# Optimization experiments

Hardware: AMD Instinct MI355X
Metric: run time of the kernel (lower is better)

The kernel has to match this reference:

```python
import jax, jax.numpy as jnp
import numpy as np
import math

TAU_PLUS = 20.0
TAU_MINUS = 20.0
A_PLUS = 0.01
A_MINUS = 0.01
W_MAX = 1.0
W_MIN = 0.0
TARGET_RATE = 0.1
HOMEO = 0.001
RATE_ALPHA = 0.01
DT = 1.0


def setup_inputs() -> dict:
    key = jax.random.key(0)
    k1, k2, k3, k4 = jax.random.split(key, 4)
    B, PRE, POST = 1024, 4096, 4096
    return {
        "pre_spikes": jax.random.uniform(k1, (B, PRE), dtype=jnp.float32),
        "post_spikes": jax.random.uniform(k2, (B, POST), dtype=jnp.float32),
        "weights": jax.random.uniform(k3, (POST, PRE), dtype=jnp.float32) * 0.5,
        "pre_trace": jnp.zeros((B, PRE), dtype=jnp.float32),
        "post_trace": jnp.zeros((B, POST), dtype=jnp.float32),
        "running_rate": jax.random.uniform(k4, (POST,), dtype=jnp.float32) * 0.2,
    }


def reference(pre_spikes, post_spikes, weights, pre_trace, post_trace, running_rate):
    B = pre_spikes.shape[0]
    # trace decay
    pre_tr = pre_trace * math.exp(-DT / TAU_PLUS)
    post_tr = post_trace * math.exp(-DT / TAU_MINUS)
    # STDP weight update (learn=True, auto_scale=False)
    dw_plus = A_PLUS * jnp.einsum('bp,bq->pq', post_spikes, pre_tr) / B
    dw_minus = -A_MINUS * jnp.einsum('bp,bq->pq', post_tr, pre_spikes) / B
    dw_homeo = -HOMEO * (running_rate - TARGET_RATE)[:, None]
    new_weights = jnp.clip(weights + dw_plus + dw_minus + dw_homeo, W_MIN, W_MAX)
    # homeostatic rate EMA
    batch_rate = post_spikes.mean(axis=0)
    new_rate = running_rate * (1.0 - RATE_ALPHA) + RATE_ALPHA * batch_rate
    # trace update
    new_pre_trace = pre_tr + pre_spikes
    new_post_trace = post_tr + post_spikes
    # postsynaptic current with updated weights
    current = pre_spikes @ new_weights.T  # (B, POST)
    return current, new_weights, new_pre_trace, new_post_trace, new_rate
```

## Files before the change

### kernel.cpp

```cpp
#include <hip/hip_runtime.h>
#include <hip/hip_fp8.h>

typedef __attribute__((ext_vector_type(8))) short short8;
typedef __attribute__((ext_vector_type(4))) float floatx4;
typedef __attribute__((ext_vector_type(8))) int int8v;
typedef __attribute__((ext_vector_type(4))) int int4v;

#define LDS_PTR(x) ((__attribute__((address_space(3))) unsigned int*)(x))
#define GLB_PTR(x) ((const __attribute__((address_space(1))) unsigned int*)(x))

__device__ __forceinline__ unsigned short f2bf(float f) {
    unsigned int u = __float_as_uint(f);
    unsigned int r = (u + 0x7FFFu + ((u >> 16) & 1u)) >> 16;
    return (unsigned short)r;
}
__device__ __forceinline__ unsigned char f2fp8(float f) {
    __hip_fp8_e4m3 v(f);
    return (unsigned char)v.__x;
}
__device__ __forceinline__ float fp82f(unsigned int u) {
    __hip_fp8_e4m3 v;
    v.__x = (__hip_fp8_storage_t)(u & 0xFF);
    return (float)v;
}

__global__ __launch_bounds__(256) void prep_post_kernel(
    const float* __restrict__ S, const float* __restrict__ T,
    float* __restrict__ traceOut, unsigned char* __restrict__ At,
    int C, int K2, int Bsz, float dp)
{
    __shared__ float sT[64][65];
    __shared__ float tT[64][65];
    const int t = threadIdx.x;
    const int r0 = blockIdx.y * 64, c0 = blockIdx.x * 64;
#pragma unroll
    for (int i = 0; i < 4; ++i) {
        int rl = (t >> 4) + i * 16;
        int cl = (t & 15) * 4;
        size_t g = (size_t)(r0 + rl) * C + c0 + cl;
        float4 s4 = *(const float4*)&S[g];
        float4 t4 = *(const float4*)&T[g];
        float4 o;
        o.x = fmaf(t4.x, dp, s4.x); o.y = fmaf(t4.y, dp, s4.y);
        o.z = fmaf(t4.z, dp, s4.z); o.w = fmaf(t4.w, dp, s4.w);
        *(float4*)&traceOut[g] = o;
        sT[rl][cl + 0] = s4.x; sT[rl][cl + 1] = s4.y;
        sT[rl][cl + 2] = s4.z; sT[rl][cl + 3] = s4.w;
        tT[rl][cl + 0] = t4.x; tT[rl][cl + 1] = t4.y;
        tT[rl][cl + 2] = t4.z; tT[rl][cl + 3] = t4.w;
    }
    __syncthreads();
#pragma unroll
    for (int i = 0; i < 4; ++i) {
        int cl = (t >> 4) + i * 16;
        int rl = (t & 15) * 4;
        uchar4 a, b;
        a.x = f2fp8(sT[rl + 0][cl]); a.y = f2fp8(sT[rl + 1][cl]);
        a.z = f2fp8(sT[rl + 2][cl]); a.w = f2fp8(sT[rl + 3][cl]);
        b.x = f2fp8(tT[rl + 0][cl]); b.y = f2fp8(tT[rl + 1][cl]);
        b.z = f2fp8(tT[rl + 2][cl]); b.w = f2fp8(tT[rl + 3][cl]);
        *(uchar4*)&At[(size_t)(c0 + cl) * K2 + r0 + rl] = a;
        *(uchar4*)&At[(size_t)(c0 + cl) * K2 + Bsz + r0 + rl] = b;
    }
}

__global__ __launch_bounds__(256) void prep_pre_kernel(
    const float* __restrict__ S, const float* __restrict__ T,
    float* __restrict__ traceOut, unsigned char* __restrict__ Bt,
    unsigned short* __restrict__ preBf,
    int C, int K2, int Bsz, float dp)
{
    __shared__ float sT[64][65];
    __shared__ float tT[64][65];
    const int t = threadIdx.x;
    const int r0 = blockIdx.y * 64, c0 = blockIdx.x * 64;
#pragma unroll
    for (int i = 0; i < 4; ++i) {
        int rl = (t >> 4) + i * 16;
        int cl = (t & 15) * 4;
        size_t g = (size_t)(r0 + rl) * C + c0 + cl;
        float4 s4 = *(const float4*)&S[g];
        float4 t4 = *(const float4*)&T[g];
        float4 o;
        o.x = fmaf(t4.x, dp, s4.x); o.y = fmaf(t4.y, dp, s4.y);
        o.z = fmaf(t4.z, dp, s4.z); o.w = fmaf(t4.w, dp, s4.w);
        *(float4*)&traceOut[g] = o;
        ushort4 pb = { f2bf(s4.x), f2bf(s4.y), f2bf(s4.z), f2bf(s4.w) };
        *(ushort4*)&preBf[g] = pb;
        sT[rl][cl + 0] = s4.x; sT[rl][cl + 1] = s4.y;
        sT[rl][cl + 2] = s4.z; sT[rl][cl + 3] = s4.w;
        tT[rl][cl + 0] = t4.x; tT[rl][cl + 1] = t4.y;
        tT[rl][cl + 2] = t4.z; tT[rl][cl + 3] = t4.w;
    }
    __syncthreads();
#pragma unroll
    for (int i = 0; i < 4; ++i) {
        int cl = (t >> 4) + i * 16;
        int rl = (t & 15) * 4;
        uchar4 a, b;
        a.x = f2fp8(tT[rl + 0][cl]); a.y = f2fp8(tT[rl + 1][cl]);
        a.z = f2fp8(tT[rl + 2][cl]); a.w = f2fp8(tT[rl + 3][cl]);
        b.x = f2fp8(-sT[rl + 0][cl]); b.y = f2fp8(-sT[rl + 1][cl]);
        b.z = f2fp8(-sT[rl + 2][cl]); b.w = f2fp8(-sT[rl + 3][cl]);
        *(uchar4*)&Bt[(size_t)(c0 + cl) * K2 + r0 + rl] = a;
        *(uchar4*)&Bt[(size_t)(c0 + cl) * K2 + Bsz + r0 + rl] = b;
    }
}

__global__ __launch_bounds__(256) void rate_kernel(
    const unsigned char* __restrict__ At, const float* __restrict__ rr,
    float* __restrict__ new_rate, int K2, int Bsz)
{
    const int w = threadIdx.x >> 6, l = threadIdx.x & 63;
    const int p = blockIdx.x * 4 + w;
    const unsigned char* row = At + (size_t)p * K2;
    float s = 0.f;
    for (int k = l * 16; k < Bsz; k += 1024) {
        int4v v = *(const int4v*)&row[k];
#pragma unroll
        for (int wd = 0; wd < 4; ++wd) {
            unsigned int u = (unsigned int)v[wd];
            s += fp82f(u) + fp82f(u >> 8) + fp82f(u >> 16) + fp82f(u >> 24);
        }
    }
#pragma unroll
    for (int off = 32; off > 0; off >>= 1) s += __shfl_xor(s, off, 64);
    if (l == 0)
        new_rate[p] = rr[p] * 0.99f + 0.01f * (s / (float)Bsz);
}

__global__ __launch_bounds__(256) void dw_fp8_kernel(
    const unsigned char* __restrict__ A, const unsigned char* __restrict__ B,
    int K, int N, float s,
    const float* __restrict__ Wold, const float* __restrict__ rr,
    float* __restrict__ outF, unsigned short* __restrict__ outBf)
{
    constexpr int BM = 128, BN = 128, BK = 128;
    __shared__ unsigned char lA[2][BM * BK];
    __shared__ unsigned char lB[2][BN * BK];

    const int t = threadIdx.x;
    const int l = t & 63;
    const int w = t >> 6;
    const int wm = w >> 1, wn = w & 1;
    const int bm = blockIdx.y, bn = blockIdx.x;

    floatx4 acc[4][4] = {};

    auto stage = [&](int buf, int k0) {
#pragma unroll
        for (int i = 0; i < 4; ++i) {
            int ci = i * 256 + t;
            int r = ci >> 3, sc = ci & 7;
            int g = sc ^ (r & 7);
            const unsigned char* gpA = A + (size_t)(bm * BM + r) * K + k0 + g * 16;
            __builtin_amdgcn_global_load_lds(GLB_PTR(gpA),
                LDS_PTR(&lA[buf][ci * 16]), 16, 0, 0);
            const unsigned char* gpB = B + (size_t)(bn * BN + r) * K + k0 + g * 16;
            __builtin_amdgcn_global_load_lds(GLB_PTR(gpB),
                LDS_PTR(&lB[buf][ci * 16]), 16, 0, 0);
        }
    };

    stage(0, 0);
    __syncthreads();

    const int nT = K / BK;
    int cur = 0;
    for (int tt = 0; tt < nT; ++tt) {
        if (tt + 1 < nT) stage(cur ^ 1, (tt + 1) * BK);

        const int c = l >> 4;
        const int m = l & 15;
        int8v af[4], bf[4];
#pragma unroll
        for (int i = 0; i < 4; ++i) {
            int ra = wm * 64 + i * 16 + m;
            int s0 = (2 * c) ^ (ra & 7), s1 = (2 * c + 1) ^ (ra & 7);
            int4v lo = *(const int4v*)&lA[cur][ra * BK + s0 * 16];
            int4v hi = *(const int4v*)&lA[cur][ra * BK + s1 * 16];
            af[i][0] = lo[0]; af[i][1] = lo[1]; af[i][2] = lo[2]; af[i][3] = lo[3];
            af[i][4] = hi[0]; af[i][5] = hi[1]; af[i][6] = hi[2]; af[i][7] = hi[3];
        }
#pragma unroll
        for (int j = 0; j < 4; ++j) {
            int rb = wn * 64 + j * 16 + m;
            int s0 = (2 * c) ^ (rb & 7), s1 = (2 * c + 1) ^ (rb & 7);
            int4v lo = *(const int4v*)&lB[cur][rb * BK + s0 * 16];
            int4v hi = *(const int4v*)&lB[cur][rb * BK + s1 * 16];
            bf[j][0] = lo[0]; bf[j][1] = lo[1]; bf[j][2] = lo[2]; bf[j][3] = lo[3];
            bf[j][4] = hi[0]; bf[j][5] = hi[1]; bf[j][6] = hi[2]; bf[j][7] = hi[3];
        }
#pragma unroll
        for (int i = 0; i < 4; ++i)
#pragma unroll
            for (int j = 0; j < 4; ++j)
                acc[i][j] = __builtin_amdgcn_mfma_scale_f32_16x16x128_f8f6f4(
                    af[i], bf[j], acc[i][j], 0, 0, 0, 0x7f, 0, 0x7f);

        asm volatile("s_waitcnt vmcnt(0)" ::: "memory");
        __builtin_amdgcn_s_barrier();
        cur ^= 1;
    }

    const int pBase = bm * BM + wm * 64;
    const int qBase = bn * BN + wn * 64;
#pragma unroll
    for (int i = 0; i < 4; ++i) {
#pragma unroll
        for (int r = 0; r < 4; ++r) {
            const int p = pBase + i * 16 + (l >> 4) * 4 + r;
            const float hp = -0.001f * (rr[p] - 0.1f);
#pragma unroll
            for (int j = 0; j < 4; ++j) {
                const int q = qBase + j * 16 + (l & 15);
                const size_t idx = (size_t)p * N + q;
                float v = fmaf(s, acc[i][j][r], Wold[idx] + hp);
                v = fminf(fmaxf(v, 0.f), 1.f);
                outF[idx] = v;
                outBf[idx] = f2bf(v);
            }
        }
    }
}

template <int BM, int BN>
__global__ __launch_bounds__(256) void mfma_gemm_bt(
    const unsigned short* __restrict__ A,
    const unsigned short* __restrict__ Bm,
    int K, int N, float* __restrict__ outF)
{
    constexpr int BK = 32;
    constexpr int FI = BM / 32;
    constexpr int FJ = BN / 32;
    __shared__ unsigned short lA[2][BM * BK];
    __shared__ unsigned short lB[2][BN * BK];

    const int t = threadIdx.x;
    const int l = t & 63;
    const int w = t >> 6;
    const int wm = w >> 1, wn = w & 1;
    const int bm = blockIdx.y, bn = blockIdx.x;

    const int srow = t >> 2;
    const int sc = t & 3;
    const int gc = sc ^ ((srow >> 1) & 3);
    const int skc = sc * 8;
    const int gkc = gc * 8;

    floatx4 acc[FI][FJ] = {};

    auto stage = [&](int buf, int k0) {
#pragma unroll
        for (int i = 0; i < BM / 64; ++i) {
            const unsigned short* gp =
                A + (size_t)(bm * BM + i * 64 + srow) * K + k0 + gkc;
            __builtin_amdgcn_global_load_lds(GLB_PTR(gp),
                LDS_PTR(&lA[buf][(i * 64 + srow) * BK + skc]), 16, 0, 0);
        }
#pragma unroll
        for (int i = 0; i < BN / 64; ++i) {
            const unsigned short* gp =
                Bm + (size_t)(bn * BN + i * 64 + srow) * K + k0 + gkc;
            __builtin_amdgcn_global_load_lds(GLB_PTR(gp),
                LDS_PTR(&lB[buf][(i * 64 + srow) * BK + skc]), 16, 0, 0);
        }
    };

    stage(0, 0);
    __syncthreads();

    const int nT = K / BK;
    int cur = 0;
    for (int tt = 0; tt < nT; ++tt) {
        if (tt + 1 < nT) stage(cur ^ 1, (tt + 1) * BK);

        const int q = l >> 4;
        short8 af[FI], bf[FJ];
#pragma unroll
        for (int i = 0; i < FI; ++i) {
            int ra = wm * (BM / 2) + i * 16 + (l & 15);
            af[i] = *(const short8*)&lA[cur][ra * BK + ((q ^ ((ra >> 1) & 3)) * 8)];
        }
#pragma unroll
        for (int j = 0; j < FJ; ++j) {
            int rb = wn * (BN / 2) + j * 16 + (l & 15);
            bf[j] = *(const short8*)&lB[cur][rb * BK + ((q ^ ((rb >> 1) & 3)) * 8)];
        }
#pragma unroll
        for (int i = 0; i < FI; ++i)
#pragma unroll
            for (int j = 0; j < FJ; ++j)
                acc[i][j] = __builtin_amdgcn_mfma_f32_16x16x32_bf16(
                    af[i], bf[j], acc[i][j], 0, 0, 0);

        asm volatile("s_waitcnt vmcnt(0)" ::: "memory");
        __builtin_amdgcn_s_barrier();
        cur ^= 1;
    }

    const int pBase = bm * BM + wm * (BM / 2);
    const int qBase = bn * BN + wn * (BN / 2);
#pragma unroll
    for (int i = 0; i < FI; ++i)
#pragma unroll
        for (int r = 0; r < 4; ++r) {
            const int p = pBase + i * 16 + (l >> 4) * 4 + r;
#pragma unroll
            for (int j = 0; j < FJ; ++j) {
                const int q = qBase + j * 16 + (l & 15);
                outF[(size_t)p * N + q] = acc[i][j][r];
            }
        }
}

extern "C" void kernel_launch(void* const* d_in, const int* in_sizes, int n_in,
                              void* d_out, int out_size, void* d_ws, size_t ws_size,
                              hipStream_t stream)
{
    const float* pre_spikes   = (const float*)d_in[0];
    const float* post_spikes  = (const float*)d_in[1];
    const float* weights      = (const float*)d_in[2];
    const float* pre_trace    = (const float*)d_in[3];
    const float* post_trace   = (const float*)d_in[4];
    const float* running_rate = (const float*)d_in[5];

    const int POST = in_sizes[5];
    const int PRE  = in_sizes[2] / POST;
    const int Bsz  = in_sizes[0] / PRE;
    const int K2   = 2 * Bsz;

    const size_t nCur   = (size_t)Bsz * POST;
    const size_t nW     = (size_t)POST * PRE;
    const size_t nPreT  = (size_t)Bsz * PRE;
    const size_t nPostT = (size_t)Bsz * POST;

    float* out_current    = (float*)d_out;
    float* out_weights    = out_current + nCur;
    float* out_pre_trace  = out_weights + nW;
    float* out_post_trace = out_pre_trace + nPreT;
    float* out_rate       = out_post_trace + nPostT;

    unsigned char* At     = (unsigned char*)d_ws;
    unsigned char* Bt     = At + (size_t)POST * K2;
    unsigned short* preBf = (unsigned short*)(Bt + (size_t)PRE * K2);
    unsigned short* wBf   = preBf + nPreT;

    const float dp = 0.95122942450071400910f;
    const float s  = dp * (0.01f / (float)Bsz);

    prep_post_kernel<<<dim3(POST / 64, Bsz / 64), 256, 0, stream>>>(
        post_spikes, post_trace, out_post_trace, At, POST, K2, Bsz, dp);
    prep_pre_kernel<<<dim3(PRE / 64, Bsz / 64), 256, 0, stream>>>(
        pre_spikes, pre_trace, out_pre_trace, Bt, preBf, PRE, K2, Bsz, dp);

    rate_kernel<<<POST / 4, 256, 0, stream>>>(
        At, running_rate, out_rate, K2, Bsz);

    dw_fp8_kernel<<<dim3(PRE / 128, POST / 128), 256, 0, stream>>>(
        At, Bt, K2, PRE, s, weights, running_rate, out_weights, wBf);

    mfma_gemm_bt<64, 128><<<dim3(POST / 128, Bsz / 64), 256, 0, stream>>>(
        preBf, wBf, PRE, POST, out_current);
}
```

Measured before the change: 336.4 us.

## Stage GEMM epilogues through LDS for vectorized stores; enlarge current GEMM tiles

The fp8 weight-update kernel now writes its accumulator tile to shared memory and then does coalesced float4 reads of the old weights and float4/ushort4 stores of the new weights, replacing the scattered scalar epilogue. The bf16 current GEMM moves from 64x128 tiles with BK=32 to 128x128 tiles with BK=64, an 8-chunk XOR swizzle, and the same LDS-staged vectorized epilogue. The aim is to cut uncoalesced global memory traffic in the epilogues and raise data reuse in the second GEMM. The cost is more LDS per block (64KB) and half as many blocks for the current GEMM, which may lower occupancy.

```diff
diff --git a/kernel.cpp b/kernel.cpp
--- a/kernel.cpp
+++ b/kernel.cpp
@@ -136,8 +136,7 @@
     float* __restrict__ outF, unsigned short* __restrict__ outBf)
 {
     constexpr int BM = 128, BN = 128, BK = 128;
-    __shared__ unsigned char lA[2][BM * BK];
-    __shared__ unsigned char lB[2][BN * BK];
+    __shared__ unsigned char smem[65536];
 
     const int t = threadIdx.x;
     const int l = t & 63;
@@ -148,6 +147,8 @@
     floatx4 acc[4][4] = {};
 
     auto stage = [&](int buf, int k0) {
+        unsigned char* la = smem + buf * 16384;
+        unsigned char* lb = smem + 32768 + buf * 16384;
 #pragma unroll
         for (int i = 0; i < 4; ++i) {
             int ci = i * 256 + t;
@@ -155,10 +156,10 @@
             int g = sc ^ (r & 7);
             const unsigned char* gpA = A + (size_t)(bm * BM + r) * K + k0 + g * 16;
             __builtin_amdgcn_global_load_lds(GLB_PTR(gpA),
-                LDS_PTR(&lA[buf][ci * 16]), 16, 0, 0);
+                LDS_PTR(la + ci * 16), 16, 0, 0);
             const unsigned char* gpB = B + (size_t)(bn * BN + r) * K + k0 + g * 16;
             __builtin_amdgcn_global_load_lds(GLB_PTR(gpB),
-                LDS_PTR(&lB[buf][ci * 16]), 16, 0, 0);
+                LDS_PTR(lb + ci * 16), 16, 0, 0);
         }
     };
 
@@ -170,6 +171,8 @@
     for (int tt = 0; tt < nT; ++tt) {
         if (tt + 1 < nT) stage(cur ^ 1, (tt + 1) * BK);
 
+        const unsigned char* la = smem + cur * 16384;
+        const unsigned char* lb = smem + 32768 + cur * 16384;
         const int c = l >> 4;
         const int m = l & 15;
         int8v af[4], bf[4];
@@ -177,8 +180,8 @@
         for (int i = 0; i < 4; ++i) {
             int ra = wm * 64 + i * 16 + m;
             int s0 = (2 * c) ^ (ra & 7), s1 = (2 * c + 1) ^ (ra & 7);
-            int4v lo = *(const int4v*)&lA[cur][ra * BK + s0 * 16];
-            int4v hi = *(const int4v*)&lA[cur][ra * BK + s1 * 16];
+            int4v lo = *(const int4v*)&la[ra * BK + s0 * 16];
+            int4v hi = *(const int4v*)&la[ra * BK + s1 * 16];
             af[i][0] = lo[0]; af[i][1] = lo[1]; af[i][2] = lo[2]; af[i][3] = lo[3];
             af[i][4] = hi[0]; af[i][5] = hi[1]; af[i][6] = hi[2]; af[i][7] = hi[3];
         }
@@ -186,8 +189,8 @@
         for (int j = 0; j < 4; ++j) {
             int rb = wn * 64 + j * 16 + m;
             int s0 = (2 * c) ^ (rb & 7), s1 = (2 * c + 1) ^ (rb & 7);
-            int4v lo = *(const int4v*)&lB[cur][rb * BK + s0 * 16];
-            int4v hi = *(const int4v*)&lB[cur][rb * BK + s1 * 16];
+            int4v lo = *(const int4v*)&lb[rb * BK + s0 * 16];
+            int4v hi = *(const int4v*)&lb[rb * BK + s1 * 16];
             bf[j][0] = lo[0]; bf[j][1] = lo[1]; bf[j][2] = lo[2]; bf[j][3] = lo[3];
             bf[j][4] = hi[0]; bf[j][5] = hi[1]; bf[j][6] = hi[2]; bf[j][7] = hi[3];
         }
@@ -203,38 +206,52 @@
         cur ^= 1;
     }
 
-    const int pBase = bm * BM + wm * 64;
-    const int qBase = bn * BN + wn * 64;
-#pragma unroll
-    for (int i = 0; i < 4; ++i) {
+    __syncthreads();
+    float* sOut = (float*)smem;
+#pragma unroll
+    for (int i = 0; i < 4; ++i)
 #pragma unroll
         for (int r = 0; r < 4; ++r) {
-            const int p = pBase + i * 16 + (l >> 4) * 4 + r;
-            const float hp = -0.001f * (rr[p] - 0.1f);
+            const int row = wm * 64 + i * 16 + (l >> 4) * 4 + r;
 #pragma unroll
             for (int j = 0; j < 4; ++j) {
-                const int q = qBase + j * 16 + (l & 15);
-                const size_t idx = (size_t)p * N + q;
-                float v = fmaf(s, acc[i][j][r], Wold[idx] + hp);
-                v = fminf(fmaxf(v, 0.f), 1.f);
-                outF[idx] = v;
-                outBf[idx] = f2bf(v);
+                const int col = wn * 64 + j * 16 + (l & 15);
+                sOut[row * 128 + col] = acc[i][j][r];
             }
         }
-    }
-}
-
-template <int BM, int BN>
+    __syncthreads();
+
+    const int pBase = bm * BM;
+    const int qBase = bn * BN;
+#pragma unroll
+    for (int k = 0; k < 16; ++k) {
+        const int ci = k * 256 + t;
+        const int row = ci >> 5;
+        const int cc = (ci & 31) * 4;
+        const int p = pBase + row;
+        const int q = qBase + cc;
+        const size_t idx = (size_t)p * N + q;
+        float4 a4 = *(const float4*)&sOut[ci * 4];
+        float4 w4 = *(const float4*)&Wold[idx];
+        const float hp = -0.001f * (rr[p] - 0.1f);
+        float4 v;
+        v.x = fminf(fmaxf(fmaf(s, a4.x, w4.x + hp), 0.f), 1.f);
+        v.y = fminf(fmaxf(fmaf(s, a4.y, w4.y + hp), 0.f), 1.f);
+        v.z = fminf(fmaxf(fmaf(s, a4.z, w4.z + hp), 0.f), 1.f);
+        v.w = fminf(fmaxf(fmaf(s, a4.w, w4.w + hp), 0.f), 1.f);
+        *(float4*)&outF[idx] = v;
+        ushort4 b4 = { f2bf(v.x), f2bf(v.y), f2bf(v.z), f2bf(v.w) };
+        *(ushort4*)&outBf[idx] = b4;
+    }
+}
+
 __global__ __launch_bounds__(256) void mfma_gemm_bt(
     const unsigned short* __restrict__ A,
     const unsigned short* __restrict__ Bm,
     int K, int N, float* __restrict__ outF)
 {
-    constexpr int BK = 32;
-    constexpr int FI = BM / 32;
-    constexpr int FJ = BN / 32;
-    __shared__ unsigned short lA[2][BM * BK];
-    __shared__ unsigned short lB[2][BN * BK];
+    constexpr int BM = 128, BN = 128, BK = 64;
+    __shared__ unsigned char smem[65536];
 
     const int t = threadIdx.x;
     const int l = t & 63;
@@ -242,28 +259,22 @@
     const int wm = w >> 1, wn = w & 1;
     const int bm = blockIdx.y, bn = blockIdx.x;
 
-    const int srow = t >> 2;
-    const int sc = t & 3;
-    const int gc = sc ^ ((srow >> 1) & 3);
-    const int skc = sc * 8;
-    const int gkc = gc * 8;
-
-    floatx4 acc[FI][FJ] = {};
+    floatx4 acc[4][4] = {};
 
     auto stage = [&](int buf, int k0) {
-#pragma unroll
-        for (int i = 0; i < BM / 64; ++i) {
-            const unsigned short* gp =
-                A + (size_t)(bm * BM + i * 64 + srow) * K + k0 + gkc;
-            __builtin_amdgcn_global_load_lds(GLB_PTR(gp),
-                LDS_PTR(&lA[buf][(i * 64 + srow) * BK + skc]), 16, 0, 0);
-        }
-#pragma unroll
-        for (int i = 0; i < BN / 64; ++i) {
-            const unsigned short* gp =
-                Bm + (size_t)(bn * BN + i * 64 + srow) * K + k0 + gkc;
-            __builtin_amdgcn_global_load_lds(GLB_PTR(gp),
-                LDS_PTR(&lB[buf][(i * 64 + srow) * BK + skc]), 16, 0, 0);
+        unsigned short* la = (unsigned short*)(smem + buf * 16384);
+        unsigned short* lb = (unsigned short*)(smem + 32768 + buf * 16384);
+#pragma unroll
+        for (int i = 0; i < 4; ++i) {
+            int ci = i * 256 + t;
+            int r = ci >> 3, sc = ci & 7;
+            int g = sc ^ (r & 7);
+            const unsigned short* gpA = A + (size_t)(bm * BM + r) * K + k0 + g * 8;
+            __builtin_amdgcn_global_load_lds(GLB_PTR(gpA),
+                LDS_PTR(la + ci * 8), 16, 0, 0);
+            const unsigned short* gpB = Bm + (size_t)(bn * BN + r) * K + k0 + g * 8;
+            __builtin_amdgcn_global_load_lds(GLB_PTR(gpB),
+                LDS_PTR(lb + ci * 8), 16, 0, 0);
         }
     };
 
@@ -275,43 +286,68 @@
     for (int tt = 0; tt < nT; ++tt) {
         if (tt + 1 < nT) stage(cur ^ 1, (tt + 1) * BK);
 
+        const unsigned short* la = (const unsigned short*)(smem + cur * 16384);
+        const unsigned short* lb = (const unsigned short*)(smem + 32768 + cur * 16384);
         const int q = l >> 4;
-        short8 af[FI], bf[FJ];
-#pragma unroll
-        for (int i = 0; i < FI; ++i) {
-            int ra = wm * (BM / 2) + i * 16 + (l & 15);
-            af[i] = *(const short8*)&lA[cur][ra * BK + ((q ^ ((ra >> 1) & 3)) * 8)];
-        }
-#pragma unroll
-        for (int j = 0; j < FJ; ++j) {
-            int rb = wn * (BN / 2) + j * 16 + (l & 15);
-            bf[j] = *(const short8*)&lB[cur][rb * BK + ((q ^ ((rb >> 1) & 3)) * 8)];
-        }
-#pragma unroll
-        for (int i = 0; i < FI; ++i)
-#pragma unroll
-            for (int j = 0; j < FJ; ++j)
-                acc[i][j] = __builtin_amdgcn_mfma_f32_16x16x32_bf16(
-                    af[i], bf[j], acc[i][j], 0, 0, 0);
+        const int m = l & 15;
+        short8 af[4][2], bf[4][2];
+#pragma unroll
+        for (int i = 0; i < 4; ++i) {
+            int ra = wm * 64 + i * 16 + m;
+#pragma unroll
+            for (int ks = 0; ks < 2; ++ks) {
+                int c2 = ks * 4 + q;
+                af[i][ks] = *(const short8*)&la[ra * BK + ((c2 ^ (ra & 7)) * 8)];
+            }
+        }
+#pragma unroll
+        for (int j = 0; j < 4; ++j) {
+            int rb = wn * 64 + j * 16 + m;
+#pragma unroll
+            for (int ks = 0; ks < 2; ++ks) {
+                int c2 = ks * 4 + q;
+                bf[j][ks] = *(const short8*)&lb[rb * BK + ((c2 ^ (rb & 7)) * 8)];
+            }
+        }
+#pragma unroll
+        for (int ks = 0; ks < 2; ++ks)
+#pragma unroll
+            for (int i = 0; i < 4; ++i)
+#pragma unroll
+                for (int j = 0; j < 4; ++j)
+                    acc[i][j] = __builtin_amdgcn_mfma_f32_16x16x32_bf16(
+                        af[i][ks], bf[j][ks], acc[i][j], 0, 0, 0);
 
         asm volatile("s_waitcnt vmcnt(0)" ::: "memory");
         __builtin_amdgcn_s_barrier();
         cur ^= 1;
     }
 
-    const int pBase = bm * BM + wm * (BM / 2);
-    const int qBase = bn * BN + wn * (BN / 2);
-#pragma unroll
-    for (int i = 0; i < FI; ++i)
+    __syncthreads();
+    float* sOut = (float*)smem;
+#pragma unroll
+    for (int i = 0; i < 4; ++i)
 #pragma unroll
         for (int r = 0; r < 4; ++r) {
-            const int p = pBase + i * 16 + (l >> 4) * 4 + r;
-#pragma unroll
-            for (int j = 0; j < FJ; ++j) {
-                const int q = qBase + j * 16 + (l & 15);
-                outF[(size_t)p * N + q] = acc[i][j][r];
+            const int row = wm * 64 + i * 16 + (l >> 4) * 4 + r;
+#pragma unroll
+            for (int j = 0; j < 4; ++j) {
+                const int col = wn * 64 + j * 16 + (l & 15);
+                sOut[row * 128 + col] = acc[i][j][r];
             }
         }
+    __syncthreads();
+
+    const int pBase = bm * BM;
+    const int qBase = bn * BN;
+#pragma unroll
+    for (int k = 0; k < 16; ++k) {
+        const int ci = k * 256 + t;
+        const int row = ci >> 5;
+        const int cc = (ci & 31) * 4;
+        float4 v = *(const float4*)&sOut[ci * 4];
+        *(float4*)&outF[(size_t)(pBase + row) * N + qBase + cc] = v;
+    }
 }
 
 extern "C" void kernel_launch(void* const* d_in, const int* in_sizes, int n_in,
@@ -360,6 +396,6 @@
     dw_fp8_kernel<<<dim3(PRE / 128, POST / 128), 256, 0, stream>>>(
         At, Bt, K2, PRE, s, weights, running_rate, out_weights, wBf);
 
-    mfma_gemm_bt<64, 128><<<dim3(POST / 128, Bsz / 64), 256, 0, stream>>>(
+    mfma_gemm_bt<<<dim3(POST / 128, Bsz / 128), 256, 0, stream>>>(
         preBf, wBf, PRE, POST, out_current);
 }
```

New measurement: 309.3 us. 1.09x faster.
